# Performance work log

Measured on AMD Instinct MI355X. Metric: run time of the kernel, lower is better.

The kernel has to match this reference:

```python
import jax, jax.numpy as jnp
import numpy as np

EPS_NORM = 1e-12  # torch F.normalize default eps
EPS_OUT = 1e-06   # module eps
CLAMP = 100.0


def setup_inputs() -> dict:
    key = jax.random.key(0)
    kq, kk = jax.random.split(key)
    B, H, S, D = 2, 16, 2048, 128
    q = jax.random.normal(kq, (B, H, S, D), dtype=jnp.float32)
    k = jax.random.normal(kk, (B, H, S, D), dtype=jnp.float32)
    log_temperature = jnp.zeros((), dtype=jnp.float32)  # log(1.0)
    return {"q": q, "k": k, "log_temperature": log_temperature}


def _l2norm(x):
    # matches torch F.normalize: x / max(||x||_2, eps)
    n = jnp.sqrt(jnp.sum(x * x, axis=-1, keepdims=True))
    return x / jnp.maximum(n, EPS_NORM)


def reference(q, k, log_temperature):
    temp = jnp.clip(jnp.exp(log_temperature), 0.05, 100.0)
    qn = _l2norm(q)
    kn = _l2norm(k)
    # (B,H,S,D) x (B,H,S,D) -> (B,H,S,S)
    scores = jnp.einsum("bhsd,bhtd->bhst", qn, kn)
    scores = jnp.clip(scores / temp, -CLAMP, CLAMP)
    kernel = jnp.exp(scores)
    return kernel + EPS_OUT
```

## Files before the change

### kernel.cpp

```cpp
#include <hip/hip_runtime.h>

#define S 2048
#define D 128
#define BH 32
#define ROWS (BH * S)

typedef __bf16 bf16x8 __attribute__((ext_vector_type(8)));
typedef float f32x4 __attribute__((ext_vector_type(4)));
typedef __attribute__((address_space(1))) unsigned int GU;
typedef __attribute__((address_space(3))) unsigned int LU;

__device__ __forceinline__ unsigned short f2bf(float f) {
  unsigned u = __float_as_uint(f);
  u += 0x7fffu + ((u >> 16) & 1u);
  return (unsigned short)(u >> 16);
}

__device__ __forceinline__ void ld_g2l16(const unsigned short* g, unsigned short* l) {
  __builtin_amdgcn_global_load_lds((const GU*)g, (LU*)l, 16, 0, 0);
}

__global__ __launch_bounds__(256) void normalize_rows(
    const float* __restrict__ x, unsigned short* __restrict__ y) {
  const int wave = threadIdx.x >> 6;
  const int lane = threadIdx.x & 63;
  const int row = (blockIdx.x << 2) + wave;
  const float2 v = ((const float2*)(x + (size_t)row * D))[lane];
  float ss = v.x * v.x + v.y * v.y;
#pragma unroll
  for (int m = 32; m; m >>= 1) ss += __shfl_xor(ss, m, 64);
  const float scale = 1.0f / fmaxf(sqrtf(ss), 1e-12f);
  const unsigned lo = f2bf(v.x * scale);
  const unsigned hi = f2bf(v.y * scale);
  ((unsigned int*)(y + (size_t)row * D))[lane] = lo | (hi << 16);
}

__global__ __launch_bounds__(256, 4) void qk_exp_kernel(
    const unsigned short* __restrict__ Qn, const unsigned short* __restrict__ Kn,
    const float* __restrict__ logt, float* __restrict__ out) {
  __shared__ __align__(16) unsigned short lK[128 * 128];
  const int tid = threadIdx.x;
  const int nt_ = blockIdx.x, mt_ = blockIdx.y, bh = blockIdx.z;
  const unsigned short* Qb = Qn + ((size_t)bh * S + (size_t)mt_ * 128) * D;
  const unsigned short* Kb = Kn + ((size_t)bh * S + (size_t)nt_ * 128) * D;

#pragma unroll
  for (int it = 0; it < 8; ++it) {
    const int L = (it << 8) + tid;
    const int r = L >> 4, c = L & 15;
    const int g = (r << 4) + (c ^ (r & 15));
    ld_g2l16(Kb + (g << 3), lK + (L << 3));
  }

  const int lane = tid & 63, wave = tid >> 6;
  const int wr = wave << 5;
  const int lm = lane & 15, kq = lane >> 4;

  const unsigned short* qrow0 = Qb + (size_t)(wr + lm) * D + (kq << 3);

  bf16x8 a0 = *(const bf16x8*)(qrow0);
  bf16x8 a1 = *(const bf16x8*)(qrow0 + (D << 4));
  __syncthreads();

  f32x4 acc[2][8] = {};
#pragma unroll
  for (int ks = 0; ks < 4; ++ks) {
    const int ksn = (ks + 1) & 3;
    bf16x8 a0n = *(const bf16x8*)(qrow0 + (ksn << 5));
    bf16x8 a1n = *(const bf16x8*)(qrow0 + (D << 4) + (ksn << 5));

    const int kc = (ks << 2) + kq;
    const int sw = (kc ^ lm) << 3;
    bf16x8 b[8];
#pragma unroll
    for (int nt = 0; nt < 8; ++nt)
      b[nt] = *(const bf16x8*)(lK + ((nt << 4) + lm) * D + sw);
#pragma unroll
    for (int nt = 0; nt < 8; ++nt) {
      acc[0][nt] = __builtin_amdgcn_mfma_f32_16x16x32_bf16(a0, b[nt], acc[0][nt], 0, 0, 0);
      acc[1][nt] = __builtin_amdgcn_mfma_f32_16x16x32_bf16(a1, b[nt], acc[1][nt], 0, 0, 0);
    }
    a0 = a0n;
    a1 = a1n;
  }

  float temp = __expf(logt[0]);
  temp = fminf(fmaxf(temp, 0.05f), 100.0f);
  const float invt = 1.0f / temp;

  float* Cb = out + ((size_t)bh << 22);
  const int rb = (mt_ << 7) + wr + (kq << 2);
  const int cb = (nt_ << 7) + lm;
#pragma unroll
  for (int mt = 0; mt < 2; ++mt) {
#pragma unroll
    for (int reg = 0; reg < 4; ++reg) {
      const int row = rb + (mt << 4) + reg;
      float* rp = Cb + (size_t)row * S + cb;
#pragma unroll
      for (int nt = 0; nt < 8; ++nt) {
        float s = acc[mt][nt][reg] * invt;
        s = fminf(fmaxf(s, -100.0f), 100.0f);
        rp[nt << 4] = __expf(s) + 1e-6f;
      }
    }
  }
}

extern "C" void kernel_launch(void* const* d_in, const int* in_sizes, int n_in,
                              void* d_out, int out_size, void* d_ws, size_t ws_size,
                              hipStream_t stream) {
  const float* q = (const float*)d_in[0];
  const float* k = (const float*)d_in[1];
  const float* lt = (const float*)d_in[2];
  float* out = (float*)d_out;
  unsigned short* qn = (unsigned short*)d_ws;
  unsigned short* kn = qn + (size_t)ROWS * D;
  normalize_rows<<<ROWS / 4, 256, 0, stream>>>(q, qn);
  normalize_rows<<<ROWS / 4, 256, 0, stream>>>(k, kn);
  dim3 grid(S / 128, S / 128, BH);
  qk_exp_kernel<<<grid, 256, 0, stream>>>(qn, kn, lt, out);
}
```

Measured before the change: 630.7 us.

## Stage output tile through LDS for coalesced 16-byte global stores

The exp results are written into a swizzled LDS buffer, now 64KB of floats reused from the K tile, and then read back so each lane issues contiguous float4 stores to global memory. Previously each lane wrote scattered 4-byte values with 64-byte strides. This targets the store-bound output write of the 512MB result. In exchange it adds an extra barrier and LDS traffic, and the larger LDS footprint lowers the launch-bounds occupancy hint from 4 to 2 blocks.

```diff
diff --git a/kernel.cpp b/kernel.cpp
--- a/kernel.cpp
+++ b/kernel.cpp
@@ -35,10 +35,12 @@
   ((unsigned int*)(y + (size_t)row * D))[lane] = lo | (hi << 16);
 }
 
-__global__ __launch_bounds__(256, 4) void qk_exp_kernel(
+__global__ __launch_bounds__(256, 2) void qk_exp_kernel(
     const unsigned short* __restrict__ Qn, const unsigned short* __restrict__ Kn,
     const float* __restrict__ logt, float* __restrict__ out) {
-  __shared__ __align__(16) unsigned short lK[128 * 128];
+  __shared__ __align__(16) float smemT[16384];
+  unsigned short* lK = (unsigned short*)smemT;
+
   const int tid = threadIdx.x;
   const int nt_ = blockIdx.x, mt_ = blockIdx.y, bh = blockIdx.z;
   const unsigned short* Qb = Qn + ((size_t)bh * S + (size_t)mt_ * 128) * D;
@@ -84,26 +86,43 @@
     a1 = a1n;
   }
 
+  __syncthreads();
+
   float temp = __expf(logt[0]);
   temp = fminf(fmaxf(temp, 0.05f), 100.0f);
   const float invt = 1.0f / temp;
 
-  float* Cb = out + ((size_t)bh << 22);
-  const int rb = (mt_ << 7) + wr + (kq << 2);
-  const int cb = (nt_ << 7) + lm;
+  float* tw = smemT + (wave << 12);
 #pragma unroll
   for (int mt = 0; mt < 2; ++mt) {
 #pragma unroll
-    for (int reg = 0; reg < 4; ++reg) {
-      const int row = rb + (mt << 4) + reg;
-      float* rp = Cb + (size_t)row * S + cb;
+    for (int nt = 0; nt < 8; ++nt) {
+      const int c = (nt << 4) + lm;
 #pragma unroll
-      for (int nt = 0; nt < 8; ++nt) {
-        float s = acc[mt][nt][reg] * invt;
-        s = fminf(fmaxf(s, -100.0f), 100.0f);
-        rp[nt << 4] = __expf(s) + 1e-6f;
+      for (int rp = 0; rp < 2; ++rp) {
+        const int lr = (mt << 4) + (kq << 2) + (rp << 1);
+        const int X = ((lr >> 1) & 7) << 2;
+        const int idx = (lr << 7) + (c ^ X);
+        float s0 = acc[mt][nt][rp * 2 + 0] * invt;
+        float s1 = acc[mt][nt][rp * 2 + 1] * invt;
+        s0 = fminf(fmaxf(s0, -100.0f), 100.0f);
+        s1 = fminf(fmaxf(s1, -100.0f), 100.0f);
+        tw[idx] = __expf(s0) + 1e-6f;
+        tw[idx + 128] = __expf(s1) + 1e-6f;
       }
     }
+  }
+
+  float* Cb = out + ((size_t)bh << 22);
+  const int l5 = lane >> 5, l31 = lane & 31;
+  const size_t gbase =
+      (size_t)((mt_ << 7) + wr) * S + (nt_ << 7) + (l31 << 2);
+#pragma unroll
+  for (int rr = 0; rr < 16; ++rr) {
+    const int lr = (rr << 1) + l5;
+    const int X = (rr & 7) << 2;
+    const f32x4 v = *(const f32x4*)(tw + (lr << 7) + (((l31 << 2)) ^ X));
+    *(f32x4*)(Cb + gbase + (size_t)lr * S) = v;
   }
 }
 
```

New measurement: 632.8 us. No clear change (+0.3%).
